# Kernel optimization log

Measured on AMD Instinct MI355X. Metric: run time of the kernel, lower is better.

The kernel has to match this reference:

```python
import jax, jax.numpy as jnp
import numpy as np

B, S, E, H, D, R = 2, 2048, 1024, 16, 64, 16


def setup_inputs() -> dict:
    key = jax.random.key(0)
    ks = jax.random.split(key, 9)
    s = lambda k, shape, fan: jax.random.normal(k, shape, dtype=jnp.float32) / np.sqrt(fan)
    return {
        "x": jax.random.normal(ks[0], (B, S, E), dtype=jnp.float32),
        "Wq": s(ks[1], (H, E, D), E),
        "bq": jnp.zeros((H, D), jnp.float32),
        "Wk": s(ks[2], (H, E, D), E),
        "bk": jnp.zeros((H, D), jnp.float32),
        "Wvd": s(ks[3], (H, E, R), E),
        "bvd": jnp.zeros((H, R), jnp.float32),
        "Wvu": s(ks[4], (H, R, D), R),
        "bvu": jnp.zeros((H, D), jnp.float32),
    }


def reference(x, Wq, bq, Wk, bk, Wvd, bvd, Wvu, bvu):
    b, s, e = x.shape
    # per-head projections, vectorized over heads h
    q = jnp.einsum('bse,hed->bhsd', x, Wq) + bq[None, :, None, :]
    k = jnp.einsum('bse,hed->bhsd', x, Wk) + bk[None, :, None, :]
    # NOTE: original scales by sqrt(embedding_dimension), not head dim
    scores = jnp.einsum('bhsd,bhtd->bhst', q, k) / jnp.sqrt(jnp.float32(e))
    # original mask: masked_fill where key_idx < query_idx (anti-causal)
    qi = jnp.arange(s)[:, None]
    ki = jnp.arange(s)[None, :]
    scores = jnp.where(ki < qi, -jnp.inf, scores)
    att = jax.nn.softmax(scores, axis=-1)  # dropout p=0 (eval)
    # low-rank value: up(down(x))
    vd = jnp.einsum('bse,her->bhsr', x, Wvd) + bvd[None, :, None, :]
    v = jnp.einsum('bhsr,hrd->bhsd', vd, Wvu) + bvu[None, :, None, :]
    out = jnp.einsum('bhst,bhtd->bhsd', att, v)
    # concat heads along last dim (head order = stack order)
    return out.transpose(0, 2, 1, 3).reshape(b, s, -1)
```

## Files before the change

### kernel.cpp

```cpp
#include <hip/hip_runtime.h>
#include <stdint.h>

#define B_ 2
#define S_ 2048
#define E_ 1024
#define H_ 16
#define D_ 64
#define R_ 16

typedef short s16x8 __attribute__((ext_vector_type(8)));
typedef float f32x4 __attribute__((ext_vector_type(4)));

#define K1_ 0.045084220027780106f
#define K0_ -28.853900817779268f

__device__ __forceinline__ unsigned short f2bf(float f) {
  union { float f; unsigned u; } v; v.f = f;
  return (unsigned short)((v.u + 0x8000u) >> 16);
}

__device__ __forceinline__ void load_lds16(const void* g, void* l) {
  __builtin_amdgcn_global_load_lds(
      (__attribute__((address_space(1))) void*)(g),
      (__attribute__((address_space(3))) void*)(l), 16, 0, 0);
}

__global__ void k_prep(const float* __restrict__ x,
                       const float* __restrict__ Wq, const float* __restrict__ Wk,
                       const float* __restrict__ Wvd, const float* __restrict__ Wvu,
                       const float* __restrict__ bq, const float* __restrict__ bk,
                       const float* __restrict__ bvd, const float* __restrict__ bvu,
                       unsigned short* __restrict__ xb, unsigned short* __restrict__ Wt,
                       float* __restrict__ ball) {
  __shared__ float T[64][65];
  const int blk = blockIdx.x;
  const int t = threadIdx.x;
  if (blk < 4096) {
    int i = (blk * 256 + t) * 4;
    float4 v = *(const float4*)(x + i);
    ushort4 o;
    o.x = f2bf(v.x); o.y = f2bf(v.y); o.z = f2bf(v.z); o.w = f2bf(v.w);
    *(ushort4*)(xb + i) = o;
  } else if (blk < 4608) {
    const int bb = blk - 4096;
    const int which = bb >> 8;
    const int h = (bb >> 4) & 15;
    const int et = bb & 15;
    const float scl = which ? 1.f : K1_;
    const float* src = (which ? Wk : Wq) + (h * E_ + et * 64) * D_;
#pragma unroll
    for (int pr = 0; pr < 4; ++pr) {
      const int row = pr * 16 + (t >> 4);
      const int col = (t & 15) * 4;
      float4 v = *(const float4*)(src + row * 64 + col);
      T[row][col] = v.x; T[row][col + 1] = v.y; T[row][col + 2] = v.z; T[row][col + 3] = v.w;
    }
    __syncthreads();
#pragma unroll
    for (int pr = 0; pr < 4; ++pr) {
      const int d = pr * 16 + (t >> 4);
      const int ec = (t & 15) * 4;
      ushort4 o;
      o.x = f2bf(T[ec][d] * scl); o.y = f2bf(T[ec + 1][d] * scl);
      o.z = f2bf(T[ec + 2][d] * scl); o.w = f2bf(T[ec + 3][d] * scl);
      *(ushort4*)(Wt + ((which << 10) + h * 64 + d) * 1024 + et * 64 + ec) = o;
    }
  } else if (blk < 8704) {
    const int idx = (blk - 4608) * 256 + t;
    const int row = idx >> 10;
    const int e = idx & 1023;
    const int h = row >> 6, d = row & 63;
    const float4* wd4 = (const float4*)(Wvd + (h << 14) + e * 16);
    const float* wu = Wvu + h * R_ * D_ + d;
    float acc = 0.f;
#pragma unroll
    for (int r4 = 0; r4 < 4; ++r4) {
      float4 a = wd4[r4];
      acc += a.x * wu[(r4 * 4 + 0) * 64];
      acc += a.y * wu[(r4 * 4 + 1) * 64];
      acc += a.z * wu[(r4 * 4 + 2) * 64];
      acc += a.w * wu[(r4 * 4 + 3) * 64];
    }
    Wt[(2048 + row) * 1024 + e] = f2bf(acc);
  } else {
    int n = (blk - 8704) * 256 + t;
    int which = n >> 10;
    int hd = n & 1023;
    int h = hd >> 6, d = hd & 63;
    float v;
    if (which == 0) v = bq[hd] * K1_;
    else if (which == 1) v = bk[hd];
    else {
      v = bvu[hd];
#pragma unroll
      for (int r = 0; r < R_; ++r) v += bvd[h * R_ + r] * Wvu[(h * R_ + r) * D_ + d];
    }
    ball[n] = v;
  }
}


__global__ __launch_bounds__(256, 3) void k_gemm_qkv(
    const unsigned short* __restrict__ X, const unsigned short* __restrict__ Wt,
    const float* __restrict__ ball,
    unsigned short* __restrict__ Qb, unsigned short* __restrict__ Kb,
    unsigned short* __restrict__ Vb) {
  __shared__ unsigned short As[128 * 32];
  __shared__ unsigned short Bs[128 * 32];
  const int tid = threadIdx.x;
  const int lane = tid & 63, wave = tid >> 6;
  const int quad = lane >> 4, l16 = lane & 15;
  const int mBase = blockIdx.y * 128, nBase = blockIdx.x * 128;
  const int wm = (wave & 1) * 64, wn = (wave >> 1) * 64;
  const int lrow = lane >> 2, lcol = (lane & 3) * 8;
  const int which = nBase >> 10;
  const bool qk = (which != 2);

  f32x4 acc[4][4];
#pragma unroll
  for (int mi = 0; mi < 4; ++mi)
#pragma unroll
    for (int ni = 0; ni < 4; ++ni) acc[mi][ni] = (f32x4){0.f, 0.f, 0.f, 0.f};

  for (int k0 = 0; k0 < E_; k0 += 32) {
#pragma unroll
    for (int i = 0; i < 2; ++i) {
      const int r0 = __builtin_amdgcn_readfirstlane((wave + i * 4) * 16);
      load_lds16(X + (mBase + r0 + lrow) * E_ + k0 + lcol, &As[r0 * 32]);
      load_lds16(Wt + (nBase + r0 + lrow) * E_ + k0 + lcol, &Bs[r0 * 32]);
    }
    __syncthreads();
    s16x8 af[4], bfr[4];
#pragma unroll
    for (int mi = 0; mi < 4; ++mi)
      af[mi] = *(const s16x8*)&As[(wm + mi * 16 + l16) * 32 + quad * 8];
#pragma unroll
    for (int ni = 0; ni < 4; ++ni)
      bfr[ni] = *(const s16x8*)&Bs[(wn + ni * 16 + l16) * 32 + quad * 8];
    if (qk) {
#pragma unroll
      for (int mi = 0; mi < 4; ++mi)
#pragma unroll
        for (int ni = 0; ni < 4; ++ni)
          acc[mi][ni] = __builtin_amdgcn_mfma_f32_16x16x32_bf16(bfr[ni], af[mi], acc[mi][ni], 0, 0, 0);
    } else {
#pragma unroll
      for (int mi = 0; mi < 4; ++mi)
#pragma unroll
        for (int ni = 0; ni < 4; ++ni)
          acc[mi][ni] = __builtin_amdgcn_mfma_f32_16x16x32_bf16(af[mi], bfr[ni], acc[mi][ni], 0, 0, 0);
    }
    __syncthreads();
  }

  if (qk) {
    unsigned short* dstBase = (which == 0) ? Qb : Kb;
#pragma unroll
    for (int mi = 0; mi < 4; ++mi) {
      const int m0 = mBase + wm + mi * 16 + l16;
      const int b = m0 >> 11;
      const int s = m0 & 2047;
#pragma unroll
      for (int ni = 0; ni < 4; ++ni) {
        const int n = nBase + wn + ni * 16 + quad * 4;
        const int nh = n & 1023;
        const int h = nh >> 6, d0 = nh & 63;
        const float4 bb = *(const float4*)&ball[n];
        const int bh = b * H_ + h;
        ushort4 pk;
        pk.x = f2bf(acc[mi][ni][0] + bb.x);
        pk.y = f2bf(acc[mi][ni][1] + bb.y);
        pk.z = f2bf(acc[mi][ni][2] + bb.z);
        pk.w = f2bf(acc[mi][ni][3] + bb.w);
        *(ushort4*)(dstBase + (bh * S_ + s) * D_ + d0) = pk;
      }
    }
  } else {
#pragma unroll
    for (int ni = 0; ni < 4; ++ni) {
      const int n = nBase + wn + ni * 16 + l16;
      const int nh = n & 1023;
      const int h = nh >> 6, d = nh & 63;
      const float bias = ball[n];
#pragma unroll
      for (int mi = 0; mi < 4; ++mi) {
        const int m0 = mBase + wm + mi * 16 + quad * 4;
        const int b = m0 >> 11;
        const int s = m0 & 2047;
        const int bh = b * H_ + h;
        ushort4 pk;
        pk.x = f2bf(acc[mi][ni][0] + bias);
        pk.y = f2bf(acc[mi][ni][1] + bias);
        pk.z = f2bf(acc[mi][ni][2] + bias);
        pk.w = f2bf(acc[mi][ni][3] + bias);
        *(ushort4*)(Vb + (bh * D_ + d) * S_ + s) = pk;
      }
    }
  }
}


__global__ __launch_bounds__(256, 4) void k_attn(
    const unsigned short* __restrict__ Qb, const unsigned short* __restrict__ Kb,
    const unsigned short* __restrict__ Vb, float* __restrict__ out) {
  __shared__ unsigned short Ks[2 * 64 * 32];
  __shared__ unsigned short Vs[2 * 64 * 32];
  __shared__ unsigned short Ps[4][2][16][40];
  const int tid = threadIdx.x;
  const int lane = tid & 63, wave = tid >> 6;
  const int quad = lane >> 4, l16 = lane & 15;
  const int chunk = blockIdx.x >> 8;
  const int j = blockIdx.x & 255;
  int qt = j >> 3;
  if (chunk & 1) qt = 31 - qt;
  const int bh = (j & 7) + 8 * chunk;
  const int q0 = qt * 64;
  const int lrow = lane >> 2, lcol = (lane & 3) * 8;
  const int r0 = __builtin_amdgcn_readfirstlane(wave * 16);
  const f32x4 kvec = {K0_, K0_, K0_, K0_};

  s16x8 qf[2];
  {
    const unsigned short* qp = Qb + (bh * S_ + q0 + wave * 16 + l16) * D_ + quad * 8;
    qf[0] = *(const s16x8*)qp;
    qf[1] = *(const s16x8*)(qp + 32);
  }
  f32x4 o[4];
#pragma unroll
  for (int dc = 0; dc < 4; ++dc) o[dc] = (f32x4){0.f, 0.f, 0.f, 0.f};
  float l_acc[4] = {0.f, 0.f, 0.f, 0.f};

  for (int kt = qt; kt < S_ / 64; ++kt) {
    const int k0 = kt * 64;
#pragma unroll
    for (int hdc = 0; hdc < 2; ++hdc) {
      load_lds16(Kb + (bh * S_ + k0 + r0 + lrow) * D_ + hdc * 32 + lcol,
                 &Ks[hdc * 2048 + r0 * 32]);
      load_lds16(Vb + (bh * D_ + r0 + lrow) * S_ + k0 + hdc * 32 + lcol,
                 &Vs[hdc * 2048 + r0 * 32]);
    }
    __syncthreads();

    f32x4 sc[4];
#pragma unroll
    for (int tc = 0; tc < 4; ++tc) {
      f32x4 a = __builtin_amdgcn_mfma_f32_16x16x32_bf16(
          qf[0], *(const s16x8*)&Ks[(tc * 16 + l16) * 32 + quad * 8], kvec, 0, 0, 0);
      sc[tc] = __builtin_amdgcn_mfma_f32_16x16x32_bf16(
          qf[1], *(const s16x8*)&Ks[2048 + (tc * 16 + l16) * 32 + quad * 8], a, 0, 0, 0);
    }

    if (kt == qt) {
#pragma unroll
      for (int tc = 0; tc < 4; ++tc)
#pragma unroll
        for (int r = 0; r < 4; ++r) {
          const int t = tc * 16 + l16;
          const int q = wave * 16 + quad * 4 + r;
          if (t < q) sc[tc][r] = -200.f;
        }
    }

#pragma unroll
    for (int tc = 0; tc < 4; ++tc)
#pragma unroll
      for (int r = 0; r < 4; ++r) {
        float p = exp2f(sc[tc][r]);
        l_acc[r] += p;
        Ps[wave][tc >> 1][quad * 4 + r][(tc & 1) * 16 + l16] =
            (unsigned short)(__float_as_uint(p) >> 16);
      }

#pragma unroll
    for (int kc = 0; kc < 2; ++kc) {
      s16x8 pf = *(const s16x8*)&Ps[wave][kc][l16][quad * 8];
#pragma unroll
      for (int dc = 0; dc < 4; ++dc) {
        s16x8 vb = *(const s16x8*)&Vs[kc * 2048 + (dc * 16 + l16) * 32 + quad * 8];
        o[dc] = __builtin_amdgcn_mfma_f32_16x16x32_bf16(pf, vb, o[dc], 0, 0, 0);
      }
    }
    __syncthreads();
  }

#pragma unroll
  for (int off = 1; off < 16; off <<= 1)
#pragma unroll
    for (int r = 0; r < 4; ++r) l_acc[r] += __shfl_xor(l_acc[r], off);
  float rinv[4];
#pragma unroll
  for (int r = 0; r < 4; ++r) rinv[r] = 1.f / l_acc[r];

  const int b = bh >> 4, h = bh & 15;
#pragma unroll
  for (int dc = 0; dc < 4; ++dc)
#pragma unroll
    for (int r = 0; r < 4; ++r) {
      const int s = q0 + wave * 16 + quad * 4 + r;
      out[(b * S_ + s) * (H_ * D_) + h * D_ + dc * 16 + l16] = o[dc][r] * rinv[r];
    }
}


extern "C" void kernel_launch(void* const* d_in, const int* in_sizes, int n_in,
                              void* d_out, int out_size, void* d_ws, size_t ws_size,
                              hipStream_t stream) {
  const float* x   = (const float*)d_in[0];
  const float* Wq  = (const float*)d_in[1];
  const float* bq  = (const float*)d_in[2];
  const float* Wk  = (const float*)d_in[3];
  const float* bk  = (const float*)d_in[4];
  const float* Wvd = (const float*)d_in[5];
  const float* bvd = (const float*)d_in[6];
  const float* Wvu = (const float*)d_in[7];
  const float* bvu = (const float*)d_in[8];
  float* out = (float*)d_out;

  char* ws = (char*)d_ws;
  unsigned short* xb   = (unsigned short*)(ws);
  unsigned short* Wt   = (unsigned short*)(ws + (8u << 20));
  float*          ball = (float*)(ws + (14u << 20));
  unsigned short* Qb   = (unsigned short*)(ws + (15u << 20));
  unsigned short* Kb   = (unsigned short*)(ws + (23u << 20));
  unsigned short* Vb   = (unsigned short*)(ws + (31u << 20));

  k_prep<<<8716, 256, 0, stream>>>(x, Wq, Wk, Wvd, Wvu, bq, bk, bvd, bvu, xb, Wt, ball);
  k_gemm_qkv<<<dim3(3072 / 128, 4096 / 128), 256, 0, stream>>>(xb, Wt, ball, Qb, Kb, Vb);
  k_attn<<<1024, 256, 0, stream>>>(Qb, Kb, Vb, out);
}
```

Measured before the change: 193.6 us.

## Double-buffer LDS tiles in QKV GEMM and attention, load V directly to registers

```diff
diff --git a/kernel.cpp b/kernel.cpp
--- a/kernel.cpp
+++ b/kernel.cpp
@@ -105,8 +105,8 @@
     const float* __restrict__ ball,
     unsigned short* __restrict__ Qb, unsigned short* __restrict__ Kb,
     unsigned short* __restrict__ Vb) {
-  __shared__ unsigned short As[128 * 32];
-  __shared__ unsigned short Bs[128 * 32];
+  __shared__ unsigned short As[2][128 * 32];
+  __shared__ unsigned short Bs[2][128 * 32];
   const int tid = threadIdx.x;
   const int lane = tid & 63, wave = tid >> 6;
   const int quad = lane >> 4, l16 = lane & 15;
@@ -122,21 +122,31 @@
 #pragma unroll
     for (int ni = 0; ni < 4; ++ni) acc[mi][ni] = (f32x4){0.f, 0.f, 0.f, 0.f};
 
+#pragma unroll
+  for (int i = 0; i < 2; ++i) {
+    const int r0 = __builtin_amdgcn_readfirstlane((wave + i * 4) * 16);
+    load_lds16(X + (mBase + r0 + lrow) * E_ + lcol, &As[0][r0 * 32]);
+    load_lds16(Wt + (nBase + r0 + lrow) * E_ + lcol, &Bs[0][r0 * 32]);
+  }
+
+  int buf = 0;
   for (int k0 = 0; k0 < E_; k0 += 32) {
-#pragma unroll
-    for (int i = 0; i < 2; ++i) {
-      const int r0 = __builtin_amdgcn_readfirstlane((wave + i * 4) * 16);
-      load_lds16(X + (mBase + r0 + lrow) * E_ + k0 + lcol, &As[r0 * 32]);
-      load_lds16(Wt + (nBase + r0 + lrow) * E_ + k0 + lcol, &Bs[r0 * 32]);
-    }
     __syncthreads();
+    if (k0 + 32 < E_) {
+#pragma unroll
+      for (int i = 0; i < 2; ++i) {
+        const int r0 = __builtin_amdgcn_readfirstlane((wave + i * 4) * 16);
+        load_lds16(X + (mBase + r0 + lrow) * E_ + k0 + 32 + lcol, &As[buf ^ 1][r0 * 32]);
+        load_lds16(Wt + (nBase + r0 + lrow) * E_ + k0 + 32 + lcol, &Bs[buf ^ 1][r0 * 32]);
+      }
+    }
     s16x8 af[4], bfr[4];
 #pragma unroll
     for (int mi = 0; mi < 4; ++mi)
-      af[mi] = *(const s16x8*)&As[(wm + mi * 16 + l16) * 32 + quad * 8];
+      af[mi] = *(const s16x8*)&As[buf][(wm + mi * 16 + l16) * 32 + quad * 8];
 #pragma unroll
     for (int ni = 0; ni < 4; ++ni)
-      bfr[ni] = *(const s16x8*)&Bs[(wn + ni * 16 + l16) * 32 + quad * 8];
+      bfr[ni] = *(const s16x8*)&Bs[buf][(wn + ni * 16 + l16) * 32 + quad * 8];
     if (qk) {
 #pragma unroll
       for (int mi = 0; mi < 4; ++mi)
@@ -150,7 +160,7 @@
         for (int ni = 0; ni < 4; ++ni)
           acc[mi][ni] = __builtin_amdgcn_mfma_f32_16x16x32_bf16(af[mi], bfr[ni], acc[mi][ni], 0, 0, 0);
     }
-    __syncthreads();
+    buf ^= 1;
   }
 
   if (qk) {
@@ -203,8 +213,7 @@
 __global__ __launch_bounds__(256, 4) void k_attn(
     const unsigned short* __restrict__ Qb, const unsigned short* __restrict__ Kb,
     const unsigned short* __restrict__ Vb, float* __restrict__ out) {
-  __shared__ unsigned short Ks[2 * 64 * 32];
-  __shared__ unsigned short Vs[2 * 64 * 32];
+  __shared__ unsigned short Ks[2][2 * 64 * 32];
   __shared__ unsigned short Ps[4][2][16][40];
   const int tid = threadIdx.x;
   const int lane = tid & 63, wave = tid >> 6;
@@ -230,24 +239,37 @@
   for (int dc = 0; dc < 4; ++dc) o[dc] = (f32x4){0.f, 0.f, 0.f, 0.f};
   float l_acc[4] = {0.f, 0.f, 0.f, 0.f};
 
+#pragma unroll
+  for (int hdc = 0; hdc < 2; ++hdc)
+    load_lds16(Kb + (bh * S_ + q0 + r0 + lrow) * D_ + hdc * 32 + lcol,
+               &Ks[0][hdc * 2048 + r0 * 32]);
+
+  int buf = 0;
   for (int kt = qt; kt < S_ / 64; ++kt) {
-    const int k0 = kt * 64;
-#pragma unroll
-    for (int hdc = 0; hdc < 2; ++hdc) {
-      load_lds16(Kb + (bh * S_ + k0 + r0 + lrow) * D_ + hdc * 32 + lcol,
-                 &Ks[hdc * 2048 + r0 * 32]);
-      load_lds16(Vb + (bh * D_ + r0 + lrow) * S_ + k0 + hdc * 32 + lcol,
-                 &Vs[hdc * 2048 + r0 * 32]);
-    }
+    s16x8 vb[2][4];
+#pragma unroll
+    for (int kc = 0; kc < 2; ++kc)
+#pragma unroll
+      for (int dc = 0; dc < 4; ++dc)
+        vb[kc][dc] = *(const s16x8*)(Vb +
+            (bh * D_ + dc * 16 + l16) * S_ + kt * 64 + kc * 32 + quad * 8);
+
     __syncthreads();
+    if (kt + 1 < S_ / 64) {
+      const int k0n = (kt + 1) * 64;
+#pragma unroll
+      for (int hdc = 0; hdc < 2; ++hdc)
+        load_lds16(Kb + (bh * S_ + k0n + r0 + lrow) * D_ + hdc * 32 + lcol,
+                   &Ks[buf ^ 1][hdc * 2048 + r0 * 32]);
+    }
 
     f32x4 sc[4];
 #pragma unroll
     for (int tc = 0; tc < 4; ++tc) {
       f32x4 a = __builtin_amdgcn_mfma_f32_16x16x32_bf16(
-          qf[0], *(const s16x8*)&Ks[(tc * 16 + l16) * 32 + quad * 8], kvec, 0, 0, 0);
+          qf[0], *(const s16x8*)&Ks[buf][(tc * 16 + l16) * 32 + quad * 8], kvec, 0, 0, 0);
       sc[tc] = __builtin_amdgcn_mfma_f32_16x16x32_bf16(
-          qf[1], *(const s16x8*)&Ks[2048 + (tc * 16 + l16) * 32 + quad * 8], a, 0, 0, 0);
+          qf[1], *(const s16x8*)&Ks[buf][2048 + (tc * 16 + l16) * 32 + quad * 8], a, 0, 0, 0);
     }
 
     if (kt == qt) {
@@ -275,12 +297,10 @@
     for (int kc = 0; kc < 2; ++kc) {
       s16x8 pf = *(const s16x8*)&Ps[wave][kc][l16][quad * 8];
 #pragma unroll
-      for (int dc = 0; dc < 4; ++dc) {
-        s16x8 vb = *(const s16x8*)&Vs[kc * 2048 + (dc * 16 + l16) * 32 + quad * 8];
-        o[dc] = __builtin_amdgcn_mfma_f32_16x16x32_bf16(pf, vb, o[dc], 0, 0, 0);
-      }
-    }
-    __syncthreads();
+      for (int dc = 0; dc < 4; ++dc)
+        o[dc] = __builtin_amdgcn_mfma_f32_16x16x32_bf16(pf, vb[kc][dc], o[dc], 0, 0, 0);
+    }
+    buf ^= 1;
   }
 
 #pragma unroll
```

New measurement: 223.8 us. 15.6% more time.

## Double-buffer K tiles and register-prefetch V in attention; unify QKV GEMM epilogue

Applied to the files above, without the earlier changes.

```diff
diff --git a/kernel.cpp b/kernel.cpp
--- a/kernel.cpp
+++ b/kernel.cpp
@@ -100,7 +100,7 @@
 }
 
 
-__global__ __launch_bounds__(256, 3) void k_gemm_qkv(
+__global__ __launch_bounds__(256, 2) void k_gemm_qkv(
     const unsigned short* __restrict__ X, const unsigned short* __restrict__ Wt,
     const float* __restrict__ ball,
     unsigned short* __restrict__ Qb, unsigned short* __restrict__ Kb,
@@ -113,8 +113,6 @@
   const int mBase = blockIdx.y * 128, nBase = blockIdx.x * 128;
   const int wm = (wave & 1) * 64, wn = (wave >> 1) * 64;
   const int lrow = lane >> 2, lcol = (lane & 3) * 8;
-  const int which = nBase >> 10;
-  const bool qk = (which != 2);
 
   f32x4 acc[4][4];
 #pragma unroll
@@ -137,63 +135,38 @@
 #pragma unroll
     for (int ni = 0; ni < 4; ++ni)
       bfr[ni] = *(const s16x8*)&Bs[(wn + ni * 16 + l16) * 32 + quad * 8];
-    if (qk) {
-#pragma unroll
-      for (int mi = 0; mi < 4; ++mi)
-#pragma unroll
-        for (int ni = 0; ni < 4; ++ni)
-          acc[mi][ni] = __builtin_amdgcn_mfma_f32_16x16x32_bf16(bfr[ni], af[mi], acc[mi][ni], 0, 0, 0);
-    } else {
-#pragma unroll
-      for (int mi = 0; mi < 4; ++mi)
-#pragma unroll
-        for (int ni = 0; ni < 4; ++ni)
-          acc[mi][ni] = __builtin_amdgcn_mfma_f32_16x16x32_bf16(af[mi], bfr[ni], acc[mi][ni], 0, 0, 0);
-    }
-    __syncthreads();
-  }
-
-  if (qk) {
-    unsigned short* dstBase = (which == 0) ? Qb : Kb;
+#pragma unroll
+    for (int mi = 0; mi < 4; ++mi)
+#pragma unroll
+      for (int ni = 0; ni < 4; ++ni)
+        acc[mi][ni] = __builtin_amdgcn_mfma_f32_16x16x32_bf16(af[mi], bfr[ni], acc[mi][ni], 0, 0, 0);
+    __syncthreads();
+  }
+
+  const int which = nBase >> 10;
+#pragma unroll
+  for (int ni = 0; ni < 4; ++ni) {
+    const int n = nBase + wn + ni * 16 + l16;
+    const int nh = n & 1023;
+    const int h = nh >> 6, d = nh & 63;
+    const float bias = ball[n];
 #pragma unroll
     for (int mi = 0; mi < 4; ++mi) {
-      const int m0 = mBase + wm + mi * 16 + l16;
+      const int m0 = mBase + wm + mi * 16 + quad * 4;
       const int b = m0 >> 11;
       const int s = m0 & 2047;
-#pragma unroll
-      for (int ni = 0; ni < 4; ++ni) {
-        const int n = nBase + wn + ni * 16 + quad * 4;
-        const int nh = n & 1023;
-        const int h = nh >> 6, d0 = nh & 63;
-        const float4 bb = *(const float4*)&ball[n];
-        const int bh = b * H_ + h;
-        ushort4 pk;
-        pk.x = f2bf(acc[mi][ni][0] + bb.x);
-        pk.y = f2bf(acc[mi][ni][1] + bb.y);
-        pk.z = f2bf(acc[mi][ni][2] + bb.z);
-        pk.w = f2bf(acc[mi][ni][3] + bb.w);
-        *(ushort4*)(dstBase + (bh * S_ + s) * D_ + d0) = pk;
-      }
-    }
-  } else {
-#pragma unroll
-    for (int ni = 0; ni < 4; ++ni) {
-      const int n = nBase + wn + ni * 16 + l16;
-      const int nh = n & 1023;
-      const int h = nh >> 6, d = nh & 63;
-      const float bias = ball[n];
-#pragma unroll
-      for (int mi = 0; mi < 4; ++mi) {
-        const int m0 = mBase + wm + mi * 16 + quad * 4;
-        const int b = m0 >> 11;
-        const int s = m0 & 2047;
-        const int bh = b * H_ + h;
+      const int bh = b * H_ + h;
+      if (which == 2) {
         ushort4 pk;
         pk.x = f2bf(acc[mi][ni][0] + bias);
         pk.y = f2bf(acc[mi][ni][1] + bias);
         pk.z = f2bf(acc[mi][ni][2] + bias);
         pk.w = f2bf(acc[mi][ni][3] + bias);
         *(ushort4*)(Vb + (bh * D_ + d) * S_ + s) = pk;
+      } else {
+        unsigned short* dst = (which == 0 ? Qb : Kb) + (bh * S_ + s) * D_ + d;
+#pragma unroll
+        for (int r = 0; r < 4; ++r) dst[r * D_] = f2bf(acc[mi][ni][r] + bias);
       }
     }
   }
@@ -203,8 +176,7 @@
 __global__ __launch_bounds__(256, 4) void k_attn(
     const unsigned short* __restrict__ Qb, const unsigned short* __restrict__ Kb,
     const unsigned short* __restrict__ Vb, float* __restrict__ out) {
-  __shared__ unsigned short Ks[2 * 64 * 32];
-  __shared__ unsigned short Vs[2 * 64 * 32];
+  __shared__ unsigned short Ks[2][2 * 64 * 32];
   __shared__ unsigned short Ps[4][2][16][40];
   const int tid = threadIdx.x;
   const int lane = tid & 63, wave = tid >> 6;
@@ -230,58 +202,91 @@
   for (int dc = 0; dc < 4; ++dc) o[dc] = (f32x4){0.f, 0.f, 0.f, 0.f};
   float l_acc[4] = {0.f, 0.f, 0.f, 0.f};
 
-  for (int kt = qt; kt < S_ / 64; ++kt) {
-    const int k0 = kt * 64;
-#pragma unroll
-    for (int hdc = 0; hdc < 2; ++hdc) {
-      load_lds16(Kb + (bh * S_ + k0 + r0 + lrow) * D_ + hdc * 32 + lcol,
-                 &Ks[hdc * 2048 + r0 * 32]);
-      load_lds16(Vb + (bh * D_ + r0 + lrow) * S_ + k0 + hdc * 32 + lcol,
-                 &Vs[hdc * 2048 + r0 * 32]);
-    }
-    __syncthreads();
-
-    f32x4 sc[4];
-#pragma unroll
-    for (int tc = 0; tc < 4; ++tc) {
-      f32x4 a = __builtin_amdgcn_mfma_f32_16x16x32_bf16(
-          qf[0], *(const s16x8*)&Ks[(tc * 16 + l16) * 32 + quad * 8], kvec, 0, 0, 0);
-      sc[tc] = __builtin_amdgcn_mfma_f32_16x16x32_bf16(
-          qf[1], *(const s16x8*)&Ks[2048 + (tc * 16 + l16) * 32 + quad * 8], a, 0, 0, 0);
-    }
-
-    if (kt == qt) {
-#pragma unroll
-      for (int tc = 0; tc < 4; ++tc)
-#pragma unroll
-        for (int r = 0; r < 4; ++r) {
-          const int t = tc * 16 + l16;
-          const int q = wave * 16 + quad * 4 + r;
-          if (t < q) sc[tc][r] = -200.f;
-        }
-    }
-
-#pragma unroll
-    for (int tc = 0; tc < 4; ++tc)
-#pragma unroll
-      for (int r = 0; r < 4; ++r) {
-        float p = exp2f(sc[tc][r]);
-        l_acc[r] += p;
-        Ps[wave][tc >> 1][quad * 4 + r][(tc & 1) * 16 + l16] =
-            (unsigned short)(__float_as_uint(p) >> 16);
-      }
-
-#pragma unroll
-    for (int kc = 0; kc < 2; ++kc) {
-      s16x8 pf = *(const s16x8*)&Ps[wave][kc][l16][quad * 8];
-#pragma unroll
-      for (int dc = 0; dc < 4; ++dc) {
-        s16x8 vb = *(const s16x8*)&Vs[kc * 2048 + (dc * 16 + l16) * 32 + quad * 8];
-        o[dc] = __builtin_amdgcn_mfma_f32_16x16x32_bf16(pf, vb, o[dc], 0, 0, 0);
-      }
-    }
-    __syncthreads();
-  }
+#define LOAD_V(kt_, vb_)                                                       \
+  {                                                                            \
+    const unsigned short* vp_ = Vb + (bh * D_ + l16) * S_ + (kt_) * 64;        \
+    _Pragma("unroll")                                                          \
+    for (int kc = 0; kc < 2; ++kc)                                             \
+      _Pragma("unroll")                                                        \
+      for (int dc = 0; dc < 4; ++dc)                                           \
+        vb_[kc][dc] = *(const s16x8*)(vp_ + (dc * 16) * S_ + kc * 32 + quad * 8); \
+  }
+
+#define DMA_K(kt_, b_)                                                         \
+  {                                                                            \
+    _Pragma("unroll")                                                          \
+    for (int hdc = 0; hdc < 2; ++hdc)                                          \
+      load_lds16(Kb + (bh * S_ + (kt_) * 64 + r0 + lrow) * D_ + hdc * 32 + lcol, \
+                 &Ks[b_][hdc * 2048 + r0 * 32]);                               \
+  }
+
+#define TILE(kt_, b_, vb_, diag_)                                              \
+  {                                                                            \
+    f32x4 sc[4];                                                               \
+    _Pragma("unroll")                                                          \
+    for (int tc = 0; tc < 4; ++tc) {                                           \
+      f32x4 a_ = __builtin_amdgcn_mfma_f32_16x16x32_bf16(                      \
+          qf[0], *(const s16x8*)&Ks[b_][(tc * 16 + l16) * 32 + quad * 8],      \
+          kvec, 0, 0, 0);                                                      \
+      sc[tc] = __builtin_amdgcn_mfma_f32_16x16x32_bf16(                        \
+          qf[1], *(const s16x8*)&Ks[b_][2048 + (tc * 16 + l16) * 32 + quad * 8], \
+          a_, 0, 0, 0);                                                        \
+    }                                                                          \
+    if (diag_) {                                                               \
+      _Pragma("unroll")                                                        \
+      for (int tc = 0; tc < 4; ++tc)                                           \
+        _Pragma("unroll")                                                      \
+        for (int r = 0; r < 4; ++r) {                                          \
+          const int t_ = tc * 16 + l16;                                        \
+          const int q_ = wave * 16 + quad * 4 + r;                             \
+          if (t_ < q_) sc[tc][r] = -200.f;                                     \
+        }                                                                      \
+    }                                                                          \
+    _Pragma("unroll")                                                          \
+    for (int tc = 0; tc < 4; ++tc)                                             \
+      _Pragma("unroll")                                                        \
+      for (int r = 0; r < 4; ++r) {                                            \
+        float p_ = exp2f(sc[tc][r]);                                           \
+        l_acc[r] += p_;                                                        \
+        Ps[wave][tc >> 1][quad * 4 + r][(tc & 1) * 16 + l16] =                 \
+            (unsigned short)(__float_as_uint(p_) >> 16);                       \
+      }                                                                        \
+    _Pragma("unroll")                                                          \
+    for (int kc = 0; kc < 2; ++kc) {                                           \
+      s16x8 pf_ = *(const s16x8*)&Ps[wave][kc][l16][quad * 8];                 \
+      _Pragma("unroll")                                                        \
+      for (int dc = 0; dc < 4; ++dc)                                           \
+        o[dc] = __builtin_amdgcn_mfma_f32_16x16x32_bf16(pf_, vb_[kc][dc],      \
+                                                        o[dc], 0, 0, 0);       \
+    }                                                                          \
+  }
+
+  s16x8 vbA[2][4], vbB[2][4];
+  DMA_K(qt, 0);
+  LOAD_V(qt, vbA);
+
+  int kt = qt;
+  while (kt + 1 < 32) {
+    __syncthreads();
+    DMA_K(kt + 1, 1);
+    LOAD_V(kt + 1, vbB);
+    TILE(kt, 0, vbA, (kt == qt));
+    __syncthreads();
+    if (kt + 2 < 32) {
+      DMA_K(kt + 2, 0);
+      LOAD_V(kt + 2, vbA);
+    }
+    TILE(kt + 1, 1, vbB, false);
+    kt += 2;
+  }
+  if (kt < 32) {
+    __syncthreads();
+    TILE(kt, 0, vbA, (kt == qt));
+  }
+
+#undef LOAD_V
+#undef DMA_K
+#undef TILE
 
 #pragma unroll
   for (int off = 1; off < 16; off <<= 1)
```

Result: slower. 222.2 us (+14.8%).

## Double-buffer K/V tiles in attention and unify QKV GEMM MFMA orientation

Applied to the files above, without the earlier changes.

```diff
diff --git a/kernel.cpp b/kernel.cpp
--- a/kernel.cpp
+++ b/kernel.cpp
@@ -100,7 +100,7 @@
 }
 
 
-__global__ __launch_bounds__(256, 3) void k_gemm_qkv(
+__global__ __launch_bounds__(256, 2) void k_gemm_qkv(
     const unsigned short* __restrict__ X, const unsigned short* __restrict__ Wt,
     const float* __restrict__ ball,
     unsigned short* __restrict__ Qb, unsigned short* __restrict__ Kb,
@@ -113,8 +113,6 @@
   const int mBase = blockIdx.y * 128, nBase = blockIdx.x * 128;
   const int wm = (wave & 1) * 64, wn = (wave >> 1) * 64;
   const int lrow = lane >> 2, lcol = (lane & 3) * 8;
-  const int which = nBase >> 10;
-  const bool qk = (which != 2);
 
   f32x4 acc[4][4];
 #pragma unroll
@@ -137,63 +135,38 @@
 #pragma unroll
     for (int ni = 0; ni < 4; ++ni)
       bfr[ni] = *(const s16x8*)&Bs[(wn + ni * 16 + l16) * 32 + quad * 8];
-    if (qk) {
-#pragma unroll
-      for (int mi = 0; mi < 4; ++mi)
-#pragma unroll
-        for (int ni = 0; ni < 4; ++ni)
-          acc[mi][ni] = __builtin_amdgcn_mfma_f32_16x16x32_bf16(bfr[ni], af[mi], acc[mi][ni], 0, 0, 0);
-    } else {
-#pragma unroll
-      for (int mi = 0; mi < 4; ++mi)
-#pragma unroll
-        for (int ni = 0; ni < 4; ++ni)
-          acc[mi][ni] = __builtin_amdgcn_mfma_f32_16x16x32_bf16(af[mi], bfr[ni], acc[mi][ni], 0, 0, 0);
-    }
+#pragma unroll
+    for (int mi = 0; mi < 4; ++mi)
+#pragma unroll
+      for (int ni = 0; ni < 4; ++ni)
+        acc[mi][ni] = __builtin_amdgcn_mfma_f32_16x16x32_bf16(af[mi], bfr[ni], acc[mi][ni], 0, 0, 0);
     __syncthreads();
   }
 
-  if (qk) {
-    unsigned short* dstBase = (which == 0) ? Qb : Kb;
+  const int which = nBase >> 10;
+#pragma unroll
+  for (int ni = 0; ni < 4; ++ni) {
+    const int n = nBase + wn + ni * 16 + l16;
+    const int nh = n & 1023;
+    const int h = nh >> 6, d = nh & 63;
+    const float bias = ball[n];
 #pragma unroll
     for (int mi = 0; mi < 4; ++mi) {
-      const int m0 = mBase + wm + mi * 16 + l16;
+      const int m0 = mBase + wm + mi * 16 + quad * 4;
       const int b = m0 >> 11;
       const int s = m0 & 2047;
-#pragma unroll
-      for (int ni = 0; ni < 4; ++ni) {
-        const int n = nBase + wn + ni * 16 + quad * 4;
-        const int nh = n & 1023;
-        const int h = nh >> 6, d0 = nh & 63;
-        const float4 bb = *(const float4*)&ball[n];
-        const int bh = b * H_ + h;
-        ushort4 pk;
-        pk.x = f2bf(acc[mi][ni][0] + bb.x);
-        pk.y = f2bf(acc[mi][ni][1] + bb.y);
-        pk.z = f2bf(acc[mi][ni][2] + bb.z);
-        pk.w = f2bf(acc[mi][ni][3] + bb.w);
-        *(ushort4*)(dstBase + (bh * S_ + s) * D_ + d0) = pk;
-      }
-    }
-  } else {
-#pragma unroll
-    for (int ni = 0; ni < 4; ++ni) {
-      const int n = nBase + wn + ni * 16 + l16;
-      const int nh = n & 1023;
-      const int h = nh >> 6, d = nh & 63;
-      const float bias = ball[n];
-#pragma unroll
-      for (int mi = 0; mi < 4; ++mi) {
-        const int m0 = mBase + wm + mi * 16 + quad * 4;
-        const int b = m0 >> 11;
-        const int s = m0 & 2047;
-        const int bh = b * H_ + h;
+      const int bh = b * H_ + h;
+      if (which == 2) {
         ushort4 pk;
         pk.x = f2bf(acc[mi][ni][0] + bias);
         pk.y = f2bf(acc[mi][ni][1] + bias);
         pk.z = f2bf(acc[mi][ni][2] + bias);
         pk.w = f2bf(acc[mi][ni][3] + bias);
         *(ushort4*)(Vb + (bh * D_ + d) * S_ + s) = pk;
+      } else {
+        unsigned short* dst = (which == 0 ? Qb : Kb) + (bh * S_ + s) * D_ + d;
+#pragma unroll
+        for (int r = 0; r < 4; ++r) dst[r * D_] = f2bf(acc[mi][ni][r] + bias);
       }
     }
   }
@@ -203,9 +176,9 @@
 __global__ __launch_bounds__(256, 4) void k_attn(
     const unsigned short* __restrict__ Qb, const unsigned short* __restrict__ Kb,
     const unsigned short* __restrict__ Vb, float* __restrict__ out) {
-  __shared__ unsigned short Ks[2 * 64 * 32];
-  __shared__ unsigned short Vs[2 * 64 * 32];
-  __shared__ unsigned short Ps[4][2][16][40];
+  __shared__ unsigned short Ks[2][2 * 64 * 32];
+  __shared__ unsigned short Vs[2][2 * 64 * 32];
+  __shared__ unsigned short Ps[4][16][40];
   const int tid = threadIdx.x;
   const int lane = tid & 63, wave = tid >> 6;
   const int quad = lane >> 4, l16 = lane & 15;
@@ -230,58 +203,60 @@
   for (int dc = 0; dc < 4; ++dc) o[dc] = (f32x4){0.f, 0.f, 0.f, 0.f};
   float l_acc[4] = {0.f, 0.f, 0.f, 0.f};
 
+#define DMA_KV(kt_, b_)                                                          \
+  {                                                                              \
+    _Pragma("unroll")                                                            \
+    for (int hdc = 0; hdc < 2; ++hdc) {                                          \
+      load_lds16(Kb + (bh * S_ + (kt_) * 64 + r0 + lrow) * D_ + hdc * 32 + lcol, \
+                 &Ks[b_][hdc * 2048 + r0 * 32]);                                 \
+      load_lds16(Vb + (bh * D_ + r0 + lrow) * S_ + (kt_) * 64 + hdc * 32 + lcol, \
+                 &Vs[b_][hdc * 2048 + r0 * 32]);                                 \
+    }                                                                            \
+  }
+
+  DMA_KV(qt, 0);
+
+  int buf = 0;
   for (int kt = qt; kt < S_ / 64; ++kt) {
-    const int k0 = kt * 64;
-#pragma unroll
-    for (int hdc = 0; hdc < 2; ++hdc) {
-      load_lds16(Kb + (bh * S_ + k0 + r0 + lrow) * D_ + hdc * 32 + lcol,
-                 &Ks[hdc * 2048 + r0 * 32]);
-      load_lds16(Vb + (bh * D_ + r0 + lrow) * S_ + k0 + hdc * 32 + lcol,
-                 &Vs[hdc * 2048 + r0 * 32]);
-    }
     __syncthreads();
-
-    f32x4 sc[4];
-#pragma unroll
-    for (int tc = 0; tc < 4; ++tc) {
-      f32x4 a = __builtin_amdgcn_mfma_f32_16x16x32_bf16(
-          qf[0], *(const s16x8*)&Ks[(tc * 16 + l16) * 32 + quad * 8], kvec, 0, 0, 0);
-      sc[tc] = __builtin_amdgcn_mfma_f32_16x16x32_bf16(
-          qf[1], *(const s16x8*)&Ks[2048 + (tc * 16 + l16) * 32 + quad * 8], a, 0, 0, 0);
-    }
-
-    if (kt == qt) {
-#pragma unroll
-      for (int tc = 0; tc < 4; ++tc)
+    if (kt + 1 < S_ / 64) DMA_KV(kt + 1, buf ^ 1);
+
+    const bool diag = (kt == qt);
+#pragma unroll
+    for (int kc = 0; kc < 2; ++kc) {
+#pragma unroll
+      for (int tcc = 0; tcc < 2; ++tcc) {
+        const int tc = kc * 2 + tcc;
+        f32x4 a = __builtin_amdgcn_mfma_f32_16x16x32_bf16(
+            qf[0], *(const s16x8*)&Ks[buf][(tc * 16 + l16) * 32 + quad * 8], kvec, 0, 0, 0);
+        f32x4 sc = __builtin_amdgcn_mfma_f32_16x16x32_bf16(
+            qf[1], *(const s16x8*)&Ks[buf][2048 + (tc * 16 + l16) * 32 + quad * 8], a, 0, 0, 0);
+        if (diag) {
+#pragma unroll
+          for (int r = 0; r < 4; ++r) {
+            const int t = tc * 16 + l16;
+            const int q = wave * 16 + quad * 4 + r;
+            if (t < q) sc[r] = -200.f;
+          }
+        }
 #pragma unroll
         for (int r = 0; r < 4; ++r) {
-          const int t = tc * 16 + l16;
-          const int q = wave * 16 + quad * 4 + r;
-          if (t < q) sc[tc][r] = -200.f;
+          float p = exp2f(sc[r]);
+          l_acc[r] += p;
+          Ps[wave][quad * 4 + r][tcc * 16 + l16] =
+              (unsigned short)(__float_as_uint(p) >> 16);
         }
-    }
-
-#pragma unroll
-    for (int tc = 0; tc < 4; ++tc)
-#pragma unroll
-      for (int r = 0; r < 4; ++r) {
-        float p = exp2f(sc[tc][r]);
-        l_acc[r] += p;
-        Ps[wave][tc >> 1][quad * 4 + r][(tc & 1) * 16 + l16] =
-            (unsigned short)(__float_as_uint(p) >> 16);
       }
-
-#pragma unroll
-    for (int kc = 0; kc < 2; ++kc) {
-      s16x8 pf = *(const s16x8*)&Ps[wave][kc][l16][quad * 8];
+      s16x8 pf = *(const s16x8*)&Ps[wave][l16][quad * 8];
 #pragma unroll
       for (int dc = 0; dc < 4; ++dc) {
-        s16x8 vb = *(const s16x8*)&Vs[kc * 2048 + (dc * 16 + l16) * 32 + quad * 8];
+        s16x8 vb = *(const s16x8*)&Vs[buf][kc * 2048 + (dc * 16 + l16) * 32 + quad * 8];
         o[dc] = __builtin_amdgcn_mfma_f32_16x16x32_bf16(pf, vb, o[dc], 0, 0, 0);
       }
     }
-    __syncthreads();
-  }
+    buf ^= 1;
+  }
+#undef DMA_KV
 
 #pragma unroll
   for (int off = 1; off < 16; off <<= 1)
```

Result: faster. 171.7 us (-11.3%).
